# Kernel optimization log

Hardware: AMD Instinct MI355X
Metric: run time of the kernel (lower is better)

The kernel has to match this reference:

```python
import jax, jax.numpy as jnp
import numpy as np

H = 512          # hidden_dim
AA = 21          # aa_num
NF = 6165        # num_features
B, N = 4, 2048   # graphs per batch, nodes per graph
LAMB = 1.0
OUT = 2


def gcn(x, adj, W, b):
    # Kipf GCN with self-loops on a (weighted) dense adjacency [B,n,n].
    n = adj.shape[-1]
    A = adj + jnp.eye(n, dtype=adj.dtype)
    d = jnp.sum(A, axis=-1)
    dinv = jax.lax.rsqrt(jnp.maximum(d, 1e-12))
    xw = x @ W                              # [B,n,Hout]
    msg = dinv[..., :, None] * (A @ (dinv[..., :, None] * xw))
    return msg + b


def hgpsl_pool(x, adj, att):
    # Node information score ||(I - D^-1 A) X||_1 (HGP-SL), top-k ratio 0.5,
    # then structure learning: row-softmax of pairwise attention + lamb*A.
    B_, n, h = x.shape
    d = jnp.sum(adj, axis=-1)
    dinv = 1.0 / jnp.maximum(d, 1.0)
    prop = (dinv[..., :, None] * adj) @ x
    score = jnp.sum(jnp.abs(x - prop), axis=-1)          # [B,n]
    k = n // 2
    _, idx = jax.lax.top_k(score, k)                     # [B,k]
    xk = jnp.take_along_axis(x, idx[:, :, None], axis=1)             # [B,k,h]
    a1 = jnp.take_along_axis(adj, idx[:, :, None], axis=1)           # [B,k,n]
    adjk = jnp.take_along_axis(a1, idx[:, None, :], axis=2)          # [B,k,k]
    # structure learning: e_ij = a^T [x_i || x_j] + lamb * A_ij
    li = xk @ att[:h]                                    # [B,k]
    lj = xk @ att[h:]                                    # [B,k]
    logits = li[:, :, None] + lj[:, None, :] + LAMB * adjk
    new_adj = jax.nn.softmax(logits, axis=-1)            # [B,k,k]
    return xk, new_adj


def readout(x):
    return jnp.concatenate([jnp.max(x, axis=1), jnp.mean(x, axis=1)], axis=-1)


def setup_inputs() -> dict:
    key = jax.random.key(0)
    ks = jax.random.split(key, 16)
    x = jax.random.normal(ks[0], (B, N, NF), dtype=jnp.float32)
    u = jax.random.uniform(ks[1], (B, N, N), dtype=jnp.float32)
    adj = (u < 0.008).astype(jnp.float32)
    adj = jnp.maximum(adj, jnp.swapaxes(adj, 1, 2))
    adj = adj * (1.0 - jnp.eye(N, dtype=jnp.float32))
    def w(k, shape):
        fan = shape[0]
        return jax.random.normal(k, shape, dtype=jnp.float32) / np.sqrt(fan)
    return {
        "x": x, "adj": adj,
        "lin1_W": w(ks[2], (NF - AA, H)), "lin1_b": jnp.zeros((H,), jnp.float32),
        "lin2_W": w(ks[3], (AA, AA)),     "lin2_b": jnp.zeros((AA,), jnp.float32),
        "conv1_W": w(ks[4], (H + AA, H)), "conv1_b": jnp.zeros((H,), jnp.float32),
        "conv2_W": w(ks[5], (H, H)),      "conv2_b": jnp.zeros((H,), jnp.float32),
        "conv3_W": w(ks[6], (H, H)),      "conv3_b": jnp.zeros((H,), jnp.float32),
        "att1": w(ks[7], (2 * H,)), "att2": w(ks[8], (2 * H,)),
        "fc1_W": w(ks[9], (2 * H, H)),    "fc1_b": jnp.zeros((H,), jnp.float32),
        "fc2_W": w(ks[10], (H, H // 2)),  "fc2_b": jnp.zeros((H // 2,), jnp.float32),
        "fc3_W": w(ks[11], (H // 2, OUT)),"fc3_b": jnp.zeros((OUT,), jnp.float32),
    }


def reference(x, adj, lin1_W, lin1_b, lin2_W, lin2_b, conv1_W, conv1_b,
              conv2_W, conv2_b, conv3_W, conv3_b, att1, att2,
              fc1_W, fc1_b, fc2_W, fc2_b, fc3_W, fc3_b):
    relu = jax.nn.relu
    x1 = relu(x[..., AA:] @ lin1_W + lin1_b)   # [B,N,H]
    x2 = relu(x[..., :AA] @ lin2_W + lin2_b)   # [B,N,AA]
    h = jnp.concatenate([x2, x1], axis=-1)     # [B,N,H+AA]
    h = relu(gcn(h, adj, conv1_W, conv1_b))
    h, adj1 = hgpsl_pool(h, adj, att1)         # N -> N/2
    r1 = readout(h)
    h = relu(gcn(h, adj1, conv2_W, conv2_b))
    h, adj2 = hgpsl_pool(h, adj1, att2)        # N/2 -> N/4
    r2 = readout(h)
    h = relu(gcn(h, adj2, conv3_W, conv3_b))
    r3 = readout(h)
    z = relu(r1) + relu(r2) + relu(r3)         # [B,2H]
    z = relu(z @ fc1_W + fc1_b)                # dropout is eval-mode identity
    z = relu(z @ fc2_W + fc2_b)
    return jax.nn.log_softmax(z @ fc3_W + fc3_b, axis=-1)
```

## Files before the change

kernel.cpp:

```cpp
#include <hip/hip_runtime.h>
#include <cstdint>
#include <cstddef>

typedef __bf16 bf16x8 __attribute__((ext_vector_type(8)));
typedef float f32x4 __attribute__((ext_vector_type(4)));

template <int MF>
__global__ __launch_bounds__(256) void gemm_mfma(
    const float* __restrict__ A, long lda, long sAb,
    const __bf16* __restrict__ Bp, long sBpb,
    float* __restrict__ C, long ldc, long sCb,
    int M, int N, int K,
    const float* __restrict__ bias,
    const float* __restrict__ rowscale,
    const float* __restrict__ addm, long sAddb, long ldadd,
    int do_relu)
{
  constexpr int BM = 32 * MF;
  constexpr int CH = MF / 2;
  constexpr int ABUF = MF * 4096;
  __shared__ __align__(16) char smem[2 * ABUF];

  const int bz = blockIdx.z;
  const float* Ab = A + (size_t)bz * sAb;
  const __bf16* Bb = Bp + (size_t)bz * sBpb;
  float* Cb = C + (size_t)bz * sCb;

  int flat = blockIdx.y * gridDim.x + blockIdx.x;
  const int nwg = gridDim.x * gridDim.y;
  if ((nwg & 7) == 0) { const int q = nwg >> 3; flat = (flat & 7) * q + (flat >> 3); }
  const int col0 = (flat / gridDim.y) * 128;
  const int row0 = (flat % gridDim.y) * BM;

  const int t = threadIdx.x;
  const int w = t >> 6, l = t & 63;
  const int l16 = l & 15, lq = l >> 4;
  const int wr = w >> 1, wc = w & 1;
  const int T = K >> 5;

  int aoff[CH]; const float* aptr[CH];
#pragma unroll
  for (int ch = 0; ch < CH; ++ch) {
    const int c = t + ch * 256;
    const int row = c >> 2, oct = c & 3;
    aoff[ch] = (row >> 4) * 1024 + (oct * 16 + (row & 15)) * 16;
    aptr[ch] = Ab + (size_t)(row0 + row) * lda + oct * 8;
  }

  const __bf16* bB[4];
#pragma unroll
  for (int nf = 0; nf < 4; ++nf)
    bB[nf] = Bb + ((size_t)((col0 >> 4) + wc * 4 + nf) * T) * 1024 + l * 8;

  f32x4 acc[MF][4];
#pragma unroll
  for (int i = 0; i < MF; ++i)
#pragma unroll
    for (int j = 0; j < 4; ++j) acc[i][j] = (f32x4){0.f, 0.f, 0.f, 0.f};

  float a0r[CH * 8], a1r[CH * 8];
  bf16x8 b0h[4], b0l[4], b1h[4], b1l[4];

#define GA(dst, K0)                                                         \
  { _Pragma("unroll") for (int ch = 0; ch < CH; ++ch) {                     \
      const float* ap = aptr[ch] + (K0);                                    \
      _Pragma("unroll") for (int i = 0; i < 8; ++i) dst[ch * 8 + i] = ap[i]; } }

#define GB(dh, dl, KT)                                                      \
  { _Pragma("unroll") for (int nf = 0; nf < 4; ++nf) {                      \
      dh[nf] = *(const bf16x8*)(bB[nf] + (size_t)(KT) * 1024);              \
      dl[nf] = *(const bf16x8*)(bB[nf] + (size_t)(KT) * 1024 + 512); } }

#define WA(buf, src)                                                        \
  { char* wb = smem + (buf) * ABUF;                                         \
    _Pragma("unroll") for (int ch = 0; ch < CH; ++ch) {                     \
      bf16x8 vh, vl;                                                        \
      _Pragma("unroll") for (int i = 0; i < 8; ++i) {                       \
        const __bf16 hh = (__bf16)src[ch * 8 + i];                          \
        vh[i] = hh; vl[i] = (__bf16)(src[ch * 8 + i] - (float)hh); }        \
      *(bf16x8*)(wb + aoff[ch]) = vh;                                       \
      *(bf16x8*)(wb + MF * 2048 + aoff[ch]) = vl; } }

#define COMPUTE(buf, bh, bl)                                                \
  { const char* rb = smem + (buf) * ABUF;                                   \
    _Pragma("unroll") for (int mf = 0; mf < MF; ++mf) {                     \
      const int fg = wr * MF + mf;                                          \
      bf16x8 fh = *(const bf16x8*)(rb + fg * 1024 + l * 16);                \
      bf16x8 fl = *(const bf16x8*)(rb + MF * 2048 + fg * 1024 + l * 16);    \
      _Pragma("unroll") for (int nf = 0; nf < 4; ++nf) {                    \
        acc[mf][nf] = __builtin_amdgcn_mfma_f32_16x16x32_bf16(fl, bh[nf], acc[mf][nf], 0, 0, 0); \
        acc[mf][nf] = __builtin_amdgcn_mfma_f32_16x16x32_bf16(fh, bl[nf], acc[mf][nf], 0, 0, 0); \
        acc[mf][nf] = __builtin_amdgcn_mfma_f32_16x16x32_bf16(fh, bh[nf], acc[mf][nf], 0, 0, 0); } } }

  GA(a0r, 0); GB(b0h, b0l, 0);
  if (T > 1) GA(a1r, 32);
  WA(0, a0r);
  __syncthreads();

  int kt = 0;
  for (; kt + 2 <= T; kt += 2) {
    if (kt + 2 < T) GA(a0r, (kt + 2) * 32);
    GB(b1h, b1l, kt + 1);
    COMPUTE(0, b0h, b0l);
    WA(1, a1r);
    __syncthreads();
    if (kt + 3 < T) GA(a1r, (kt + 3) * 32);
    if (kt + 2 < T) GB(b0h, b0l, kt + 2);
    COMPUTE(1, b1h, b1l);
    if (kt + 2 < T) WA(0, a0r);
    __syncthreads();
  }
  if (kt < T) {
    COMPUTE(0, b0h, b0l);
  }
#undef GA
#undef GB
#undef WA
#undef COMPUTE

#pragma unroll
  for (int mf = 0; mf < MF; ++mf) {
#pragma unroll
    for (int r = 0; r < 4; ++r) {
      const int row = row0 + wr * (MF * 16) + mf * 16 + lq * 4 + r;
      const float rs = rowscale ? rowscale[(size_t)bz * M + row] : 1.f;
#pragma unroll
      for (int nf = 0; nf < 4; ++nf) {
        const int col = col0 + wc * 64 + nf * 16 + l16;
        float v = acc[mf][nf][r];
        if (addm) v += addm[(size_t)bz * sAddb + (size_t)row * ldadd + col];
        v *= rs;
        if (bias) v += bias[col];
        if (do_relu) v = fmaxf(v, 0.f);
        Cb[(size_t)row * ldc + col] = v;
      }
    }
  }
}

__global__ __launch_bounds__(64) void pack_b_kernel(
    const float* __restrict__ in, long sInb, int Kin, int Nin,
    __bf16* __restrict__ outP, long sPb, int T)
{
  const int kt = blockIdx.x, nf = blockIdx.y, b = blockIdx.z;
  const int l = threadIdx.x;
  const float* src = in + (size_t)b * sInb;
  const int col = nf * 16 + (l & 15);
  const int k0 = kt * 32 + (l >> 4) * 8;
  bf16x8 vh, vl;
#pragma unroll
  for (int j = 0; j < 8; ++j) {
    const int k = k0 + j;
    const float v = (k < Kin) ? src[(size_t)k * Nin + col] : 0.f;
    const __bf16 h = (__bf16)v;
    vh[j] = h; vl[j] = (__bf16)(v - (float)h);
  }
  __bf16* dst = outP + (size_t)b * sPb + ((size_t)nf * T + kt) * 1024 + l * 8;
  *(bf16x8*)dst = vh;
  *(bf16x8*)(dst + 512) = vl;
}

__global__ void lin2_kernel(const float* __restrict__ x, const float* __restrict__ W,
                            const float* __restrict__ b, float* __restrict__ h)
{
  int id = blockIdx.x * blockDim.x + threadIdx.x;
  if (id >= 4 * 2048 * 21) return;
  int row = id / 21, j = id % 21;
  const float* xr = x + (size_t)row * 6165;
  float acc = b[j];
  for (int i = 0; i < 21; ++i) acc = fmaf(xr[i], W[i * 21 + j], acc);
  h[(size_t)row * 544 + j] = fmaxf(acc, 0.f);
}

__global__ void pad_h_kernel(float* __restrict__ h)
{
  int id = blockIdx.x * blockDim.x + threadIdx.x;
  if (id >= 4 * 2048 * 11) return;
  int row = id / 11, c = 533 + id % 11;
  h[(size_t)row * 544 + c] = 0.f;
}

__global__ __launch_bounds__(256) void degrees_kernel(const float* __restrict__ adj,
                                                      float* __restrict__ dg,
                                                      float* __restrict__ dp)
{
  __shared__ float red[256];
  const int row = blockIdx.x;
  const int t = threadIdx.x;
  const float* ar = adj + (size_t)row * 2048;
  float s = 0.f;
  for (int j = t; j < 2048; j += 256) s += ar[j];
  red[t] = s; __syncthreads();
  for (int off = 128; off > 0; off >>= 1) {
    if (t < off) red[t] += red[t + off];
    __syncthreads();
  }
  if (t == 0) {
    float S = red[0];
    dg[row] = rsqrtf(fmaxf(S + 1.f, 1e-12f));
    dp[row] = 1.f / fmaxf(S, 1.f);
  }
}

__global__ __launch_bounds__(256) void conv1_msg_kernel(
    const float* __restrict__ adj, const float* __restrict__ xw,
    const float* __restrict__ dinv, const float* __restrict__ bias,
    float* __restrict__ out)
{
  __shared__ int nbr[2048];
  __shared__ float nval[2048];
  __shared__ int cnts[256];
  const int b = blockIdx.y, i = blockIdx.x, t = threadIdx.x;
  const float* ar = adj + ((size_t)(b * 2048 + i)) * 2048;
  int myj[8]; float myv[8]; int mc = 0;
  const int j0 = t * 8;
#pragma unroll
  for (int q = 0; q < 8; ++q) {
    float v = ar[j0 + q];
    if (v != 0.f) { myj[mc] = j0 + q; myv[mc] = v; ++mc; }
  }
  cnts[t] = mc; __syncthreads();
  for (int off = 1; off < 256; off <<= 1) {
    int v = cnts[t]; int add = (t >= off) ? cnts[t - off] : 0;
    __syncthreads();
    cnts[t] = v + add; __syncthreads();
  }
  const int base = cnts[t] - mc;
  const int total = cnts[255];
  for (int q = 0; q < mc; ++q) { nbr[base + q] = myj[q]; nval[base + q] = myv[q]; }
  __syncthreads();

  const float* xwb = xw + (size_t)b * 2048 * 512;
  const float* dv = dinv + b * 2048;
  float acc0 = 0.f, acc1 = 0.f;
  for (int n = 0; n < total; ++n) {
    const int j = nbr[n];
    const float w = nval[n] * dv[j];
    const float* xr = xwb + (size_t)j * 512;
    acc0 = fmaf(w, xr[t], acc0);
    acc1 = fmaf(w, xr[t + 256], acc1);
  }
  const float di = dv[i];
  const float* xi = xwb + (size_t)i * 512;
  acc0 = fmaf(di, xi[t], acc0);
  acc1 = fmaf(di, xi[t + 256], acc1);
  float* orow = out + ((size_t)(b * 2048 + i)) * 512;
  orow[t]       = fmaxf(di * acc0 + bias[t], 0.f);
  orow[t + 256] = fmaxf(di * acc1 + bias[t + 256], 0.f);
}

__global__ __launch_bounds__(256) void pool1_score_kernel(
    const float* __restrict__ adj, const float* __restrict__ h1,
    const float* __restrict__ dpool, float* __restrict__ score)
{
  __shared__ int nbr[2048];
  __shared__ float nval[2048];
  __shared__ int cnts[256];
  __shared__ float red[256];
  const int b = blockIdx.y, i = blockIdx.x, t = threadIdx.x;
  const float* ar = adj + ((size_t)(b * 2048 + i)) * 2048;
  int myj[8]; float myv[8]; int mc = 0;
  const int j0 = t * 8;
#pragma unroll
  for (int q = 0; q < 8; ++q) {
    float v = ar[j0 + q];
    if (v != 0.f) { myj[mc] = j0 + q; myv[mc] = v; ++mc; }
  }
  cnts[t] = mc; __syncthreads();
  for (int off = 1; off < 256; off <<= 1) {
    int v = cnts[t]; int add = (t >= off) ? cnts[t - off] : 0;
    __syncthreads();
    cnts[t] = v + add; __syncthreads();
  }
  const int base = cnts[t] - mc;
  const int total = cnts[255];
  for (int q = 0; q < mc; ++q) { nbr[base + q] = myj[q]; nval[base + q] = myv[q]; }
  __syncthreads();

  const float* hb = h1 + (size_t)b * 2048 * 512;
  float acc0 = 0.f, acc1 = 0.f;
  for (int n = 0; n < total; ++n) {
    const int j = nbr[n];
    const float w = nval[n];
    const float* xr = hb + (size_t)j * 512;
    acc0 = fmaf(w, xr[t], acc0);
    acc1 = fmaf(w, xr[t + 256], acc1);
  }
  const float dpi = dpool[b * 2048 + i];
  const float* hi = hb + (size_t)i * 512;
  float part = fabsf(hi[t] - dpi * acc0) + fabsf(hi[t + 256] - dpi * acc1);
  red[t] = part; __syncthreads();
  for (int off = 128; off > 0; off >>= 1) {
    if (t < off) red[t] += red[t + off];
    __syncthreads();
  }
  if (t == 0) score[b * 2048 + i] = red[0];
}

__global__ __launch_bounds__(1024) void topk_kernel(
    const float* __restrict__ score, int* __restrict__ idx_out, int n, int k)
{
  __shared__ unsigned long long key[2048];
  const unsigned b = blockIdx.x, t = threadIdx.x;
  const unsigned bd = blockDim.x;
  for (unsigned i = t; i < (unsigned)n; i += bd) {
    unsigned u = __float_as_uint(score[(size_t)b * n + i]);
    key[i] = ((unsigned long long)u << 32) | (unsigned)(~i);
  }
  __syncthreads();
  for (unsigned size = 2; size <= (unsigned)n; size <<= 1) {
    for (unsigned stride = size >> 1; stride > 0; stride >>= 1) {
      const unsigned i = (t / stride) * (stride * 2) + (t % stride);
      const unsigned ixj = i + stride;
      const bool up = ((i & size) == 0);
      unsigned long long a = key[i], c = key[ixj];
      if (up ? (a < c) : (a > c)) { key[i] = c; key[ixj] = a; }
      __syncthreads();
    }
  }
  const unsigned my = ~(unsigned)(key[t] & 0xFFFFFFFFull);
  __syncthreads();
  unsigned* arr = (unsigned*)key;
  arr[t] = my;
  __syncthreads();
  for (unsigned size = 2; size <= (unsigned)k; size <<= 1) {
    for (unsigned stride = size >> 1; stride > 0; stride >>= 1) {
      if (t < (unsigned)k / 2) {
        const unsigned i = (t / stride) * (stride * 2) + (t % stride);
        const unsigned ixj = i + stride;
        const bool up = ((i & size) == 0);
        unsigned a = arr[i], c = arr[ixj];
        if (up ? (a > c) : (a < c)) { arr[i] = c; arr[ixj] = a; }
      }
      __syncthreads();
    }
  }
  idx_out[(size_t)b * k + t] = (int)arr[t];
}

__global__ __launch_bounds__(256) void gather_li_kernel(
    const float* __restrict__ X, int src_n,
    const int* __restrict__ idx, int k,
    const float* __restrict__ att,
    float* __restrict__ xk, float* __restrict__ li, float* __restrict__ lj)
{
  __shared__ float redA[256], redB[256];
  const int b = blockIdx.y, r = blockIdx.x, t = threadIdx.x;
  const int g = idx[(size_t)b * k + r];
  const float* src = X + ((size_t)(b * src_n + g)) * 512;
  float* dst = xk + ((size_t)(b * k + r)) * 512;
  const float v0 = src[t], v1 = src[t + 256];
  dst[t] = v0; dst[t + 256] = v1;
  redA[t] = v0 * att[t] + v1 * att[t + 256];
  redB[t] = v0 * att[512 + t] + v1 * att[512 + t + 256];
  __syncthreads();
  for (int off = 128; off > 0; off >>= 1) {
    if (t < off) { redA[t] += redA[t + off]; redB[t] += redB[t + off]; }
    __syncthreads();
  }
  if (t == 0) { li[(size_t)b * k + r] = redA[0]; lj[(size_t)b * k + r] = redB[0]; }
}

__global__ __launch_bounds__(256) void slearn_kernel(
    const float* __restrict__ Asrc, int src_n,
    const int* __restrict__ idx, int k,
    const float* __restrict__ li, const float* __restrict__ lj,
    float* __restrict__ adj_out, float* __restrict__ dg, float* __restrict__ dp)
{
  __shared__ int gidx[1024];
  __shared__ float ljv[1024];
  __shared__ float lg[1024];
  __shared__ float red[256];
  const int b = blockIdx.y, r = blockIdx.x, t = threadIdx.x;
  for (int j = t; j < k; j += 256) { gidx[j] = idx[(size_t)b * k + j]; ljv[j] = lj[(size_t)b * k + j]; }
  __syncthreads();
  const int gi = gidx[r];
  const float lir = li[(size_t)b * k + r];
  const float* ar = Asrc + ((size_t)(b * src_n + gi)) * src_n;
  float mx = -3.4e38f;
  for (int j = t; j < k; j += 256) {
    float v = lir + ljv[j] + ar[gidx[j]];
    lg[j] = v; mx = fmaxf(mx, v);
  }
  red[t] = mx; __syncthreads();
  for (int off = 128; off > 0; off >>= 1) {
    if (t < off) red[t] = fmaxf(red[t], red[t + off]);
    __syncthreads();
  }
  const float m = red[0]; __syncthreads();
  float sm = 0.f;
  for (int j = t; j < k; j += 256) { float e = expf(lg[j] - m); lg[j] = e; sm += e; }
  red[t] = sm; __syncthreads();
  for (int off = 128; off > 0; off >>= 1) {
    if (t < off) red[t] += red[t + off];
    __syncthreads();
  }
  const float s = red[0]; __syncthreads();
  const float inv = 1.f / s;
  float ps = 0.f;
  float* orow = adj_out + ((size_t)(b * k + r)) * k;
  for (int j = t; j < k; j += 256) { float p = lg[j] * inv; orow[j] = p; ps += p; }
  red[t] = ps; __syncthreads();
  for (int off = 128; off > 0; off >>= 1) {
    if (t < off) red[t] += red[t + off];
    __syncthreads();
  }
  if (t == 0) {
    float S = red[0];
    dg[(size_t)b * k + r] = rsqrtf(fmaxf(S + 1.f, 1e-12f));
    dp[(size_t)b * k + r] = 1.f / fmaxf(S, 1.f);
  }
}

__global__ __launch_bounds__(512) void absdiff_kernel(
    const float* __restrict__ X, const float* __restrict__ P, float* __restrict__ score)
{
  __shared__ float red[512];
  const int row = blockIdx.x, t = threadIdx.x;
  float d = fabsf(X[(size_t)row * 512 + t] - P[(size_t)row * 512 + t]);
  red[t] = d; __syncthreads();
  for (int off = 256; off > 0; off >>= 1) {
    if (t < off) red[t] += red[t + off];
    __syncthreads();
  }
  if (t == 0) score[row] = red[0];
}

__global__ __launch_bounds__(512) void readout_part_kernel(
    const float* __restrict__ X, int nrows, int chunk_rows,
    float* __restrict__ partM, float* __restrict__ partS)
{
  const int b = blockIdx.x, chunk = blockIdx.y, c = threadIdx.x;
  const float* xb = X + ((size_t)b * nrows + (size_t)chunk * chunk_rows) * 512;
  float mx = -3.4e38f, sm = 0.f;
  for (int r = 0; r < chunk_rows; ++r) {
    float v = xb[(size_t)r * 512 + c];
    mx = fmaxf(mx, v); sm += v;
  }
  const size_t o = ((size_t)(b * gridDim.y + chunk)) * 512 + c;
  partM[o] = mx; partS[o] = sm;
}

__global__ __launch_bounds__(512) void readout_comb_kernel(
    const float* __restrict__ partM, const float* __restrict__ partS,
    int nchunks, int nrows, float* __restrict__ out)
{
  const int b = blockIdx.x, c = threadIdx.x;
  float mx = -3.4e38f, sm = 0.f;
  for (int q = 0; q < nchunks; ++q) {
    const size_t o = ((size_t)(b * nchunks + q)) * 512 + c;
    mx = fmaxf(mx, partM[o]); sm += partS[o];
  }
  out[(size_t)b * 1024 + c] = mx;
  out[(size_t)b * 1024 + 512 + c] = sm / (float)nrows;
}

__global__ __launch_bounds__(512) void final_mlp_kernel(
    const float* __restrict__ r1, const float* __restrict__ r2, const float* __restrict__ r3,
    const float* __restrict__ fc1W, const float* __restrict__ fc1b,
    const float* __restrict__ fc2W, const float* __restrict__ fc2b,
    const float* __restrict__ fc3W, const float* __restrict__ fc3b,
    float* __restrict__ out)
{
  __shared__ float z[1024];
  __shared__ float z1[512];
  __shared__ float z2[256];
  __shared__ float l[2];
  const int b = blockIdx.x, t = threadIdx.x;
  for (int c = t; c < 1024; c += 512)
    z[c] = fmaxf(r1[(size_t)b * 1024 + c], 0.f) + fmaxf(r2[(size_t)b * 1024 + c], 0.f)
         + fmaxf(r3[(size_t)b * 1024 + c], 0.f);
  __syncthreads();
  {
    float acc = fc1b[t];
    for (int i = 0; i < 1024; ++i) acc = fmaf(z[i], fc1W[(size_t)i * 512 + t], acc);
    z1[t] = fmaxf(acc, 0.f);
  }
  __syncthreads();
  if (t < 256) {
    float acc = fc2b[t];
    for (int i = 0; i < 512; ++i) acc = fmaf(z1[i], fc2W[(size_t)i * 256 + t], acc);
    z2[t] = fmaxf(acc, 0.f);
  }
  __syncthreads();
  if (t < 2) {
    float acc = fc3b[t];
    for (int i = 0; i < 256; ++i) acc = fmaf(z2[i], fc3W[(size_t)i * 2 + t], acc);
    l[t] = acc;
  }
  __syncthreads();
  if (t == 0) {
    float m = fmaxf(l[0], l[1]);
    float ls = m + logf(expf(l[0] - m) + expf(l[1] - m));
    out[b * 2 + 0] = l[0] - ls;
    out[b * 2 + 1] = l[1] - ls;
  }
}

extern "C" void kernel_launch(void* const* d_in, const int* in_sizes, int n_in,
                              void* d_out, int out_size, void* d_ws, size_t ws_size,
                              hipStream_t stream)
{
  (void)in_sizes; (void)n_in; (void)out_size; (void)ws_size;
  const float* x       = (const float*)d_in[0];
  const float* adj     = (const float*)d_in[1];
  const float* lin1_W  = (const float*)d_in[2];
  const float* lin1_b  = (const float*)d_in[3];
  const float* lin2_W  = (const float*)d_in[4];
  const float* lin2_b  = (const float*)d_in[5];
  const float* conv1_W = (const float*)d_in[6];
  const float* conv1_b = (const float*)d_in[7];
  const float* conv2_W = (const float*)d_in[8];
  const float* conv2_b = (const float*)d_in[9];
  const float* conv3_W = (const float*)d_in[10];
  const float* conv3_b = (const float*)d_in[11];
  const float* att1    = (const float*)d_in[12];
  const float* att2    = (const float*)d_in[13];
  const float* fc1_W   = (const float*)d_in[14];
  const float* fc1_b   = (const float*)d_in[15];
  const float* fc2_W   = (const float*)d_in[16];
  const float* fc2_b   = (const float*)d_in[17];
  const float* fc3_W   = (const float*)d_in[18];
  const float* fc3_b   = (const float*)d_in[19];
  float* ws  = (float*)d_ws;
  float* out = (float*)d_out;

  float* h     = ws + 0;
  float* adj1  = ws + 0;
  float* xw    = ws + 4456448;
  float* prop2 = xw;
  float* xk2   = ws + 4456448 + 2097152;
  float* adj2  = ws + 4456448 + 3145728;
  float* h1    = ws + 8650752;
  float* xk1   = ws + 12845056;
  float* xw3   = xk1;
  float* h3    = ws + 12845056 + 1048576;
  float* xw2   = ws + 14942208;
  float* h2    = ws + 17039360;
  float* S     = ws + 19136512;
  float* dinv_g1 = S;
  float* dinv_p1 = S + 8192;
  float* score1  = S + 16384;
  int*   idx1    = (int*)(S + 24576);
  float* li1     = S + 28672;
  float* lj1     = S + 32768;
  float* r1      = S + 36864;
  float* dinv_g2 = S + 40960;
  float* dinv_p2 = S + 45056;
  float* score2  = S + 49152;
  int*   idx2    = (int*)(S + 53248);
  float* li2     = S + 55296;
  float* lj2     = S + 57344;
  float* r2      = S + 59392;
  float* dinv_g3 = S + 63488;
  float* dinv_p3 = S + 65536;
  float* r3      = S + 67584;

  float* partM = ws + 4718592;
  float* partS = ws + 4718592 + 32768;

  __bf16* l1P  = (__bf16*)(ws + 8650752);
  __bf16* c1P  = (__bf16*)(ws + 12845056);
  __bf16* c2P  = (__bf16*)(ws + 17039360);
  __bf16* c3P  = (__bf16*)(ws + 4456448);
  __bf16* xw2P = (__bf16*)(ws + 12845056);
  __bf16* h2P  = (__bf16*)(ws + 8650752);
  __bf16* xw3P = (__bf16*)(ws + 10747904);

  pack_b_kernel<<<dim3(192, 32, 1), 64, 0, stream>>>(lin1_W, 0, 6144, 512, l1P, 0, 192);
  pack_b_kernel<<<dim3(17, 32, 1), 64, 0, stream>>>(conv1_W, 0, 533, 512, c1P, 0, 17);
  pack_b_kernel<<<dim3(16, 32, 1), 64, 0, stream>>>(conv2_W, 0, 512, 512, c2P, 0, 16);
  lin2_kernel<<<(4 * 2048 * 21 + 255) / 256, 256, 0, stream>>>(x, lin2_W, lin2_b, h);
  pad_h_kernel<<<(4 * 2048 * 11 + 255) / 256, 256, 0, stream>>>(h);
  gemm_mfma<2><<<dim3(4, 128, 1), 256, 0, stream>>>(x + 21, 6165, 0, l1P, 0,
      h + 21, 544, 0, 8192, 512, 6144, lin1_b, nullptr, nullptr, 0, 0, 1);
  degrees_kernel<<<8192, 256, 0, stream>>>(adj, dinv_g1, dinv_p1);
  gemm_mfma<2><<<dim3(4, 128, 1), 256, 0, stream>>>(h, 544, 0, c1P, 0,
      xw, 512, 0, 8192, 512, 544, nullptr, nullptr, nullptr, 0, 0, 0);
  conv1_msg_kernel<<<dim3(2048, 4), 256, 0, stream>>>(adj, xw, dinv_g1, conv1_b, h1);
  pool1_score_kernel<<<dim3(2048, 4), 256, 0, stream>>>(adj, h1, dinv_p1, score1);
  topk_kernel<<<4, 1024, 0, stream>>>(score1, idx1, 2048, 1024);
  gather_li_kernel<<<dim3(1024, 4), 256, 0, stream>>>(h1, 2048, idx1, 1024, att1, xk1, li1, lj1);
  slearn_kernel<<<dim3(1024, 4), 256, 0, stream>>>(adj, 2048, idx1, 1024, li1, lj1, adj1, dinv_g2, dinv_p2);
  readout_part_kernel<<<dim3(4, 16), 512, 0, stream>>>(xk1, 1024, 64, partM, partS);
  readout_comb_kernel<<<4, 512, 0, stream>>>(partM, partS, 16, 1024, r1);
  gemm_mfma<2><<<dim3(4, 64, 1), 256, 0, stream>>>(xk1, 512, 0, c2P, 0,
      xw2, 512, 0, 4096, 512, 512, nullptr, dinv_g2, nullptr, 0, 0, 0);
  pack_b_kernel<<<dim3(32, 32, 4), 64, 0, stream>>>(xw2, 524288, 1024, 512, xw2P, 1048576, 32);
  gemm_mfma<2><<<dim3(4, 16, 4), 256, 0, stream>>>(adj1, 1024, 1048576, xw2P, 1048576,
      h2, 512, 524288, 1024, 512, 1024, conv2_b, dinv_g2, xw2, 524288, 512, 1);
  pack_b_kernel<<<dim3(32, 32, 4), 64, 0, stream>>>(h2, 524288, 1024, 512, h2P, 1048576, 32);
  gemm_mfma<2><<<dim3(4, 16, 4), 256, 0, stream>>>(adj1, 1024, 1048576, h2P, 1048576,
      prop2, 512, 524288, 1024, 512, 1024, nullptr, dinv_p2, nullptr, 0, 0, 0);
  absdiff_kernel<<<4096, 512, 0, stream>>>(h2, prop2, score2);
  pack_b_kernel<<<dim3(16, 32, 1), 64, 0, stream>>>(conv3_W, 0, 512, 512, c3P, 0, 16);
  topk_kernel<<<4, 512, 0, stream>>>(score2, idx2, 1024, 512);
  gather_li_kernel<<<dim3(512, 4), 256, 0, stream>>>(h2, 1024, idx2, 512, att2, xk2, li2, lj2);
  slearn_kernel<<<dim3(512, 4), 256, 0, stream>>>(adj1, 1024, idx2, 512, li2, lj2, adj2, dinv_g3, dinv_p3);
  readout_part_kernel<<<dim3(4, 16), 512, 0, stream>>>(xk2, 512, 32, partM, partS);
  readout_comb_kernel<<<4, 512, 0, stream>>>(partM, partS, 16, 512, r2);
  gemm_mfma<2><<<dim3(4, 32, 1), 256, 0, stream>>>(xk2, 512, 0, c3P, 0,
      xw3, 512, 0, 2048, 512, 512, nullptr, dinv_g3, nullptr, 0, 0, 0);
  pack_b_kernel<<<dim3(16, 32, 4), 64, 0, stream>>>(xw3, 262144, 512, 512, xw3P, 524288, 16);
  gemm_mfma<2><<<dim3(4, 8, 4), 256, 0, stream>>>(adj2, 512, 262144, xw3P, 524288,
      h3, 512, 262144, 512, 512, 512, conv3_b, dinv_g3, xw3, 262144, 512, 1);
  readout_part_kernel<<<dim3(4, 16), 512, 0, stream>>>(h3, 512, 32, partM, partS);
  readout_comb_kernel<<<4, 512, 0, stream>>>(partM, partS, 16, 512, r3);
  final_mlp_kernel<<<4, 512, 0, stream>>>(r1, r2, r3, fc1_W, fc1_b, fc2_W, fc2_b,
                                          fc3_W, fc3_b, out);
}
```

Measured before the change: 788.4 us.

## Stage B tiles through shared memory and switch to row-major tile rasterization

```diff
diff --git a/kernel.cpp b/kernel.cpp
--- a/kernel.cpp
+++ b/kernel.cpp
@@ -4,6 +4,8 @@
 
 typedef __bf16 bf16x8 __attribute__((ext_vector_type(8)));
 typedef float f32x4 __attribute__((ext_vector_type(4)));
+
+#define BUFSZ 24576
 
 template <int MF>
 __global__ __launch_bounds__(256) void gemm_mfma(
@@ -17,9 +19,7 @@
     int do_relu)
 {
   constexpr int BM = 32 * MF;
-  constexpr int CH = MF / 2;
-  constexpr int ABUF = MF * 4096;
-  __shared__ __align__(16) char smem[2 * ABUF];
+  __shared__ __align__(16) char smem[2 * BUFSZ];
 
   const int bz = blockIdx.z;
   const float* Ab = A + (size_t)bz * sAb;
@@ -29,8 +29,8 @@
   int flat = blockIdx.y * gridDim.x + blockIdx.x;
   const int nwg = gridDim.x * gridDim.y;
   if ((nwg & 7) == 0) { const int q = nwg >> 3; flat = (flat & 7) * q + (flat >> 3); }
-  const int col0 = (flat / gridDim.y) * 128;
-  const int row0 = (flat % gridDim.y) * BM;
+  const int col0 = (flat % gridDim.x) * 128;
+  const int row0 = (flat / gridDim.x) * BM;
 
   const int t = threadIdx.x;
   const int w = t >> 6, l = t & 63;
@@ -38,19 +38,17 @@
   const int wr = w >> 1, wc = w & 1;
   const int T = K >> 5;
 
-  int aoff[CH]; const float* aptr[CH];
-#pragma unroll
-  for (int ch = 0; ch < CH; ++ch) {
-    const int c = t + ch * 256;
-    const int row = c >> 2, oct = c & 3;
-    aoff[ch] = (row >> 4) * 1024 + (oct * 16 + (row & 15)) * 16;
-    aptr[ch] = Ab + (size_t)(row0 + row) * lda + oct * 8;
-  }
-
-  const __bf16* bB[4];
-#pragma unroll
-  for (int nf = 0; nf < 4; ++nf)
-    bB[nf] = Bb + ((size_t)((col0 >> 4) + wc * 4 + nf) * T) * 1024 + l * 8;
+  const int s_row = t >> 2, s_oct = t & 3;
+  const int a_off = (s_row >> 4) * 1024 + (s_oct * 16 + (s_row & 15)) * 16;
+  const float* aptr = Ab + (size_t)(row0 + s_row) * lda + s_oct * 8;
+
+  const __bf16* bsrc[4];
+#pragma unroll
+  for (int j = 0; j < 4; ++j) {
+    const int c = t + 256 * j;
+    const int g = c >> 7;
+    bsrc[j] = Bb + ((size_t)((col0 >> 4) + g) * T) * 1024 + (size_t)(c & 127) * 8;
+  }
 
   f32x4 acc[MF][4];
 #pragma unroll
@@ -58,64 +56,71 @@
 #pragma unroll
     for (int j = 0; j < 4; ++j) acc[i][j] = (f32x4){0.f, 0.f, 0.f, 0.f};
 
-  float a0r[CH * 8], a1r[CH * 8];
-  bf16x8 b0h[4], b0l[4], b1h[4], b1l[4];
+  float a0r[8], a1r[8];
+  bf16x8 bs0[4], bs1[4];
 
 #define GA(dst, K0)                                                         \
-  { _Pragma("unroll") for (int ch = 0; ch < CH; ++ch) {                     \
-      const float* ap = aptr[ch] + (K0);                                    \
-      _Pragma("unroll") for (int i = 0; i < 8; ++i) dst[ch * 8 + i] = ap[i]; } }
-
-#define GB(dh, dl, KT)                                                      \
-  { _Pragma("unroll") for (int nf = 0; nf < 4; ++nf) {                      \
-      dh[nf] = *(const bf16x8*)(bB[nf] + (size_t)(KT) * 1024);              \
-      dl[nf] = *(const bf16x8*)(bB[nf] + (size_t)(KT) * 1024 + 512); } }
+  { const float* ap = aptr + (K0);                                          \
+    _Pragma("unroll") for (int i = 0; i < 8; ++i) dst[i] = ap[i]; }
+
+#define GB(dst, KT)                                                         \
+  { _Pragma("unroll") for (int j = 0; j < 4; ++j)                           \
+      dst[j] = *(const bf16x8*)(bsrc[j] + (size_t)(KT) * 1024); }
 
 #define WA(buf, src)                                                        \
-  { char* wb = smem + (buf) * ABUF;                                         \
-    _Pragma("unroll") for (int ch = 0; ch < CH; ++ch) {                     \
-      bf16x8 vh, vl;                                                        \
-      _Pragma("unroll") for (int i = 0; i < 8; ++i) {                       \
-        const __bf16 hh = (__bf16)src[ch * 8 + i];                          \
-        vh[i] = hh; vl[i] = (__bf16)(src[ch * 8 + i] - (float)hh); }        \
-      *(bf16x8*)(wb + aoff[ch]) = vh;                                       \
-      *(bf16x8*)(wb + MF * 2048 + aoff[ch]) = vl; } }
-
-#define COMPUTE(buf, bh, bl)                                                \
-  { const char* rb = smem + (buf) * ABUF;                                   \
+  { char* wb = smem + (buf) * BUFSZ; bf16x8 vh, vl;                         \
+    _Pragma("unroll") for (int i = 0; i < 8; ++i) {                         \
+      const __bf16 hh = (__bf16)src[i];                                     \
+      vh[i] = hh; vl[i] = (__bf16)(src[i] - (float)hh); }                   \
+    *(bf16x8*)(wb + a_off) = vh;                                            \
+    *(bf16x8*)(wb + 4096 + a_off) = vl; }
+
+#define WB(buf, src)                                                        \
+  { char* wb = smem + (buf) * BUFSZ + 8192;                                 \
+    _Pragma("unroll") for (int j = 0; j < 4; ++j)                           \
+      *(bf16x8*)(wb + (t + 256 * j) * 16) = src[j]; }
+
+#define COMPUTE(buf)                                                        \
+  { const char* rb = smem + (buf) * BUFSZ;                                  \
+    bf16x8 fbh[4], fbl[4];                                                  \
+    _Pragma("unroll") for (int nf = 0; nf < 4; ++nf) {                      \
+      const int g = wc * 4 + nf;                                            \
+      fbh[nf] = *(const bf16x8*)(rb + 8192 + g * 2048 + l * 16);            \
+      fbl[nf] = *(const bf16x8*)(rb + 8192 + g * 2048 + 1024 + l * 16); }   \
     _Pragma("unroll") for (int mf = 0; mf < MF; ++mf) {                     \
       const int fg = wr * MF + mf;                                          \
       bf16x8 fh = *(const bf16x8*)(rb + fg * 1024 + l * 16);                \
-      bf16x8 fl = *(const bf16x8*)(rb + MF * 2048 + fg * 1024 + l * 16);    \
+      bf16x8 fl = *(const bf16x8*)(rb + 4096 + fg * 1024 + l * 16);         \
       _Pragma("unroll") for (int nf = 0; nf < 4; ++nf) {                    \
-        acc[mf][nf] = __builtin_amdgcn_mfma_f32_16x16x32_bf16(fl, bh[nf], acc[mf][nf], 0, 0, 0); \
-        acc[mf][nf] = __builtin_amdgcn_mfma_f32_16x16x32_bf16(fh, bl[nf], acc[mf][nf], 0, 0, 0); \
-        acc[mf][nf] = __builtin_amdgcn_mfma_f32_16x16x32_bf16(fh, bh[nf], acc[mf][nf], 0, 0, 0); } } }
-
-  GA(a0r, 0); GB(b0h, b0l, 0);
+        acc[mf][nf] = __builtin_amdgcn_mfma_f32_16x16x32_bf16(fl, fbh[nf], acc[mf][nf], 0, 0, 0); \
+        acc[mf][nf] = __builtin_amdgcn_mfma_f32_16x16x32_bf16(fh, fbl[nf], acc[mf][nf], 0, 0, 0); \
+        acc[mf][nf] = __builtin_amdgcn_mfma_f32_16x16x32_bf16(fh, fbh[nf], acc[mf][nf], 0, 0, 0); } } }
+
+  GA(a0r, 0); GB(bs0, 0);
+  WA(0, a0r); WB(0, bs0);
   if (T > 1) GA(a1r, 32);
-  WA(0, a0r);
   __syncthreads();
 
   int kt = 0;
   for (; kt + 2 <= T; kt += 2) {
     if (kt + 2 < T) GA(a0r, (kt + 2) * 32);
-    GB(b1h, b1l, kt + 1);
-    COMPUTE(0, b0h, b0l);
-    WA(1, a1r);
+    GB(bs1, kt + 1);
+    COMPUTE(0);
+    WA(1, a1r); WB(1, bs1);
     __syncthreads();
     if (kt + 3 < T) GA(a1r, (kt + 3) * 32);
-    if (kt + 2 < T) GB(b0h, b0l, kt + 2);
-    COMPUTE(1, b1h, b1l);
-    if (kt + 2 < T) WA(0, a0r);
+    if (kt + 2 < T) GB(bs0, kt + 2);
+    COMPUTE(1);
+    if (kt + 2 < T) { WA(0, a0r); WB(0, bs0); }
     __syncthreads();
   }
   if (kt < T) {
-    COMPUTE(0, b0h, b0l);
+    COMPUTE(0);
   }
 #undef GA
 #undef GB
 #undef WA
+#undef WB
 #undef COMPUTE
 
 #pragma unroll
```

Result: faster. 731.6 us (-7.2%).
